# Optimization experiments

Hardware: AMD Instinct MI355X
Metric: run time of the kernel (lower is better)

Reference implementation:

```python
import jax, jax.numpy as jnp
import numpy as np


def setup_inputs() -> dict:
    key = jax.random.key(0)
    k1, k2 = jax.random.split(key)
    B, Lc, Lm, D = 8, 2048, 2048, 128
    context = jax.random.normal(k1, (B, Lc, D), dtype=jnp.float32)
    main = jax.random.normal(k2, (B, Lm, D), dtype=jnp.float32)
    return {"context": context, "main": main}


def reference(context, main):
    # weights[b,c,m] = sum_d context[b,c,d] * main[b,m,d]   (Keras dot axes=[2,2])
    weights = jnp.einsum("bcd,bmd->bcm", context, main)
    # K.softmax default axis=-1: normalize over the main-length axis m
    weights = jax.nn.softmax(weights, axis=-1)
    # dot([weights, context], axes=1): contract axis 1 (c) of both -> (B, Lm, D)
    weighted = jnp.einsum("bcm,bcd->bmd", weights, context)
    return main - weighted
```

## Files before the change

kernel.cpp:

```cpp
#include <hip/hip_runtime.h>


#define BATCH 8
#define L_SEQ 2048
#define DD 128
#define SHIFT 40.0f
#define LDA 136

typedef __attribute__((ext_vector_type(8))) short bf16x8;
typedef __attribute__((ext_vector_type(4))) short bf16x4;
typedef __attribute__((ext_vector_type(4))) float f32x4;
typedef __attribute__((ext_vector_type(16))) float f32x16;
typedef __attribute__((ext_vector_type(4))) unsigned int uint4v;

__device__ __forceinline__ short f2bf(float f) {
    unsigned u = __builtin_bit_cast(unsigned, f);
    return (short)((u + 0x8000u) >> 16);
}

__device__ __forceinline__ void gl2lds16(const short* g, short* l) {
    __builtin_amdgcn_global_load_lds(
        (const __attribute__((address_space(1))) unsigned int*)g,
        (__attribute__((address_space(3))) unsigned int*)l, 16, 0, 0);
}

__device__ __forceinline__ void waitv8() { asm volatile("s_waitcnt vmcnt(8)" ::: "memory"); }
__device__ __forceinline__ void waitv4() { asm volatile("s_waitcnt vmcnt(4)" ::: "memory"); }
__device__ __forceinline__ void waitv0() { asm volatile("s_waitcnt vmcnt(0)" ::: "memory"); }

template <int NT>
__device__ __forceinline__ void stage_tile(short* __restrict__ dst,
                                           const float* __restrict__ src,
                                           int nelts, int t) {
    for (int base = 0; base < nelts; base += NT * 8) {
        int flat = base + t * 8;
        const float4* p = (const float4*)(src + flat);
        float4 v0 = p[0];
        float4 v1 = p[1];
        bf16x8 s;
        s[0] = f2bf(v0.x); s[1] = f2bf(v0.y); s[2] = f2bf(v0.z); s[3] = f2bf(v0.w);
        s[4] = f2bf(v1.x); s[5] = f2bf(v1.y); s[6] = f2bf(v1.z); s[7] = f2bf(v1.w);
        int row = flat >> 7;
        int col = flat & 127;
        *(bf16x8*)&dst[row * LDA + col] = s;
    }
}

__global__ __launch_bounds__(256) void zero_kernel(float* __restrict__ p, int n) {
    int i = blockIdx.x * 256 + threadIdx.x;
    if (i < n) p[i] = 0.0f;
}


__global__ __launch_bounds__(256) void convert_kernel(const float* __restrict__ ctx,
                                                      const float* __restrict__ mn,
                                                      short* __restrict__ Cbf,
                                                      short* __restrict__ Mbf,
                                                      float* __restrict__ Lg) {
    int tid = blockIdx.x * 256 + threadIdx.x;
    if (tid < BATCH * L_SEQ) Lg[tid] = 0.0f;
    const int half = BATCH * L_SEQ * DD / 8;
    int id = tid;
    const float* src;
    short* dst;
    if (id < half) { src = ctx; dst = Cbf; }
    else           { id -= half; src = mn; dst = Mbf; }
    int row = id >> 4;
    int lc = id & 15;
    const float4* p = (const float4*)(src + ((size_t)row << 7) + lc * 8);
    float4 v0 = p[0];
    float4 v1 = p[1];
    bf16x8 s;
    s[0] = f2bf(v0.x); s[1] = f2bf(v0.y); s[2] = f2bf(v0.z); s[3] = f2bf(v0.w);
    s[4] = f2bf(v1.x); s[5] = f2bf(v1.y); s[6] = f2bf(v1.z); s[7] = f2bf(v1.w);
    int pc = (lc & 8) | ((lc ^ row) & 7);
    *(bf16x8*)&dst[((size_t)row << 7) + pc * 8] = s;
}

__global__ __launch_bounds__(256, 2) void stats_kernel(const short* __restrict__ Cbf,
                                                       const short* __restrict__ Mbf,
                                                       float* __restrict__ Lg) {
    __shared__ short Cs[128 * 128];
    __shared__ short Ms[2][64 * 128];

    int bid = blockIdx.x;
    int b  = bid & 7;
    int r2 = bid >> 3;
    int mc = r2 & 3;
    int ct = r2 >> 2;
    int t = threadIdx.x;
    int w = t >> 6;
    int l = t & 63;
    int a15 = l & 15;
    int q = l >> 4;
    int h = a15 & 7;
    int cw = (w & 1) * 64;
    int mw = (w >> 1) * 32;

    const short* gC = Cbf + ((size_t)(b * L_SEQ + ct * 128)) * DD;
    const short* gM = Mbf + ((size_t)(b * L_SEQ + mc * 512)) * DD;

    {
        #pragma unroll
        for (int ii = 0; ii < 8; ++ii) {
            int inst = w * 8 + ii;
            gl2lds16(gC + inst * 512 + l * 8, Cs + inst * 512);
        }
        #pragma unroll
        for (int ii = 0; ii < 4; ++ii) {
            int inst = w * 4 + ii;
            gl2lds16(gM + inst * 512 + l * 8, Ms[0] + inst * 512);
        }
        #pragma unroll
        for (int ii = 0; ii < 4; ++ii) {
            int inst = w * 4 + ii;
            gl2lds16(gM + (size_t)64 * DD + inst * 512 + l * 8, Ms[1] + inst * 512);
        }
    }

    waitv8();
    __builtin_amdgcn_s_barrier();
    __builtin_amdgcn_sched_barrier(0);

    bf16x8 af[4][4];
    #pragma unroll
    for (int ks = 0; ks < 4; ++ks) {
        int aoff = ((ks * 4 + q) ^ h) * 8;
        #pragma unroll
        for (int i = 0; i < 4; ++i)
            af[ks][i] = *(const bf16x8*)&Cs[(cw + i * 16 + a15) * 128 + aoff];
    }

    float ls[4][4] = {};

    for (int ms = 0; ms < 8; ++ms) {
        int bp = ms & 1;
        if (ms < 7) waitv4(); else waitv0();
        __builtin_amdgcn_s_barrier();
        __builtin_amdgcn_sched_barrier(0);

        f32x4 acc[4][2];
        #pragma unroll
        for (int i = 0; i < 4; ++i)
            #pragma unroll
            for (int j = 0; j < 2; ++j) {
                f32x4 z = {0.f, 0.f, 0.f, 0.f};
                acc[i][j] = z;
            }
        #pragma unroll
        for (int ks = 0; ks < 4; ++ks) {
            int aoff = ((ks * 4 + q) ^ h) * 8;
            bf16x8 bv[2];
            #pragma unroll
            for (int j = 0; j < 2; ++j)
                bv[j] = *(const bf16x8*)&Ms[bp][(mw + j * 16 + a15) * 128 + aoff];
            #pragma unroll
            for (int i = 0; i < 4; ++i)
                #pragma unroll
                for (int j = 0; j < 2; ++j)
                    acc[i][j] = __builtin_amdgcn_mfma_f32_16x16x32_bf16(af[ks][i], bv[j], acc[i][j], 0, 0, 0);
        }

        #pragma unroll
        for (int j = 0; j < 2; ++j)
            #pragma unroll
            for (int i = 0; i < 4; ++i)
                #pragma unroll
                for (int r = 0; r < 4; ++r)
                    ls[i][r] += __expf(acc[i][j][r] - SHIFT);

        __builtin_amdgcn_s_barrier();
        __builtin_amdgcn_sched_barrier(0);
        if (ms + 2 < 8) {
            #pragma unroll
            for (int ii = 0; ii < 4; ++ii) {
                int inst = w * 4 + ii;
                gl2lds16(gM + (size_t)(ms + 2) * 64 * DD + inst * 512 + l * 8,
                         Ms[bp] + inst * 512);
            }
        }
    }

    #pragma unroll
    for (int i = 0; i < 4; ++i)
        #pragma unroll
        for (int r = 0; r < 4; ++r) {
            float v = ls[i][r];
            v += __shfl_xor(v, 1);
            v += __shfl_xor(v, 2);
            v += __shfl_xor(v, 4);
            v += __shfl_xor(v, 8);
            ls[i][r] = v;
        }
    if (a15 == 0) {
        #pragma unroll
        for (int i = 0; i < 4; ++i) {
            int c = ct * 128 + cw + i * 16 + q * 4;
            #pragma unroll
            for (int r = 0; r < 4; ++r)
                atomicAdd(&Lg[(size_t)b * L_SEQ + c + r], ls[i][r]);
        }
    }
}

__global__ __launch_bounds__(256) void prep_kernel(const float* __restrict__ ctx,
                                                   const float* __restrict__ Lg,
                                                   short* __restrict__ CtL) {
    __shared__ short Ts[128 * LDA];
    __shared__ float invLs[128];

    int b = blockIdx.x >> 4;
    int cc = blockIdx.x & 15;
    int t = threadIdx.x;

    if (t < 128) invLs[t] = 1.0f / Lg[(size_t)b * L_SEQ + cc * 128 + t];
    __syncthreads();

    const float* src = ctx + ((size_t)(b * L_SEQ + cc * 128)) * DD;
    #pragma unroll
    for (int i = 0; i < 8; ++i) {
        int flat = i * 2048 + t * 8;
        int r = flat >> 7;
        int c = flat & 127;
        const float4* p = (const float4*)(src + flat);
        float4 v0 = p[0];
        float4 v1 = p[1];
        float il = invLs[r];
        bf16x8 s;
        s[0] = f2bf(v0.x * il); s[1] = f2bf(v0.y * il); s[2] = f2bf(v0.z * il); s[3] = f2bf(v0.w * il);
        s[4] = f2bf(v1.x * il); s[5] = f2bf(v1.y * il); s[6] = f2bf(v1.z * il); s[7] = f2bf(v1.w * il);
        *(bf16x8*)&Ts[r * LDA + c] = s;
    }
    __syncthreads();

    int d = t >> 1;
    int ch = (t & 1) * 64;
    int key = d & 7;
    #pragma unroll
    for (int i = 0; i < 8; ++i) {
        int c = ch + i * 8;
        bf16x8 v;
        #pragma unroll
        for (int j = 0; j < 8; ++j) v[j] = Ts[(c + j) * LDA + d];
        int pc = cc * 16 + (ch >> 3) + (i ^ key);
        *(bf16x8*)&CtL[((size_t)(b * DD + d)) * L_SEQ + pc * 8] = v;
    }
}

__global__ __launch_bounds__(512, 2) void attend_fused(const short* __restrict__ Cbf,
                                                       const short* __restrict__ Mbf,
                                                       const short* __restrict__ CtL,
                                                       const float* __restrict__ mn,
                                                       float* __restrict__ out) {
    __shared__ __align__(16) char smem[131072];

    int bid = blockIdx.x;
    int b = bid & 7;
    int mtile = bid >> 3;
    int t = threadIdx.x;
    int w = t >> 6;
    int l = t & 63;
    int la = l & 31;
    int hi = l >> 5;
    int mg = w >> 2;
    int ch = w & 3;

    int m_glob = mtile * 64 + mg * 32 + la;
    int key7 = la & 7;

    bf16x8 mf[8];
    {
        const short* mrow = Mbf + ((size_t)(b * L_SEQ + m_glob)) * DD;
        #pragma unroll
        for (int ks = 0; ks < 8; ++ks) {
            int lc = ks * 2 + hi;
            int pc = (lc & 8) | ((lc ^ key7) & 7);
            mf[ks] = *(const bf16x8*)&mrow[pc * 8];
        }
    }

    auto stage = [&](int cs, int p) {
        short* Cw = (short*)(smem + p * 65536);
        short* Tw = (short*)(smem + p * 65536 + 32768);
        const short* gC = Cbf + ((size_t)(b * L_SEQ + cs * 128)) * DD;
        #pragma unroll
        for (int ii = 0; ii < 4; ++ii) {
            int inst = w * 4 + ii;
            gl2lds16(gC + inst * 512 + l * 8, Cw + inst * 512);
        }
        const short* gT = CtL + (size_t)b * DD * L_SEQ + (size_t)cs * 128;
        #pragma unroll
        for (int ii = 0; ii < 4; ++ii) {
            int inst = w * 4 + ii;
            int row = inst * 4 + (l >> 4);
            gl2lds16(gT + (size_t)row * L_SEQ + (l & 15) * 8, Tw + inst * 512);
        }
    };

    f32x16 o[4];
    #pragma unroll
    for (int dg = 0; dg < 4; ++dg)
        #pragma unroll
        for (int r = 0; r < 16; ++r) o[dg][r] = 0.0f;

    stage(0, 0);
    stage(1, 1);

    for (int cs = 0; cs < 16; ++cs) {
        int p = cs & 1;
        if (cs < 15) waitv8(); else waitv0();
        __builtin_amdgcn_s_barrier();
        __builtin_amdgcn_sched_barrier(0);

        const short* Cw = (const short*)(smem + p * 65536);
        const short* Tw = (const short*)(smem + p * 65536 + 32768);

        f32x16 s;
        #pragma unroll
        for (int r = 0; r < 16; ++r) s[r] = 0.0f;
        int crow = ch * 32 + la;
        #pragma unroll
        for (int ks = 0; ks < 8; ++ks) {
            int lc = ks * 2 + hi;
            int pc = (lc & 8) | ((lc ^ key7) & 7);
            bf16x8 av = *(const bf16x8*)&Cw[crow * 128 + pc * 8];
            s = __builtin_amdgcn_mfma_f32_32x32x16_bf16(av, mf[ks], s, 0, 0, 0);
        }

        unsigned u[4][2];
        #pragma unroll
        for (int q = 0; q < 4; ++q)
            #pragma unroll
            for (int jj = 0; jj < 2; ++jj) {
                float e0 = __expf(s[q * 4 + jj * 2]     - SHIFT);
                float e1 = __expf(s[q * 4 + jj * 2 + 1] - SHIFT);
                u[q][jj] = ((unsigned)(unsigned short)f2bf(e1) << 16)
                         |  (unsigned)(unsigned short)f2bf(e0);
            }

        bf16x8 pa[2];
        #pragma unroll
        for (int ks2 = 0; ks2 < 2; ++ks2) {
            unsigned a0 = u[2 * ks2][0],     a1 = u[2 * ks2][1];
            unsigned b0 = u[2 * ks2 + 1][0], b1 = u[2 * ks2 + 1][1];
            unsigned a0p = (unsigned)__shfl_xor((int)a0, 32);
            unsigned a1p = (unsigned)__shfl_xor((int)a1, 32);
            unsigned b0p = (unsigned)__shfl_xor((int)b0, 32);
            unsigned b1p = (unsigned)__shfl_xor((int)b1, 32);
            uint4v pw;
            pw.x = hi ? b0p : a0;
            pw.y = hi ? b1p : a1;
            pw.z = hi ? b0  : a0p;
            pw.w = hi ? b1  : a1p;
            pa[ks2] = __builtin_bit_cast(bf16x8, pw);
        }

        #pragma unroll
        for (int dg = 0; dg < 4; ++dg) {
            int drow = dg * 32 + la;
            #pragma unroll
            for (int ks2 = 0; ks2 < 2; ++ks2) {
                int lc2 = ch * 4 + ks2 * 2 + hi;
                int pc2 = (lc2 & 8) | ((lc2 ^ key7) & 7);
                bf16x8 tv = *(const bf16x8*)&Tw[drow * 128 + pc2 * 8];
                o[dg] = __builtin_amdgcn_mfma_f32_32x32x16_bf16(tv, pa[ks2], o[dg], 0, 0, 0);
            }
        }

        __builtin_amdgcn_s_barrier();
        __builtin_amdgcn_sched_barrier(0);
        if (cs + 2 < 16) stage(cs + 2, p);
    }

    __syncthreads();
    float* red = (float*)smem;
    {
        float* base = red + w * 4096;
        #pragma unroll
        for (int dg = 0; dg < 4; ++dg)
            #pragma unroll
            for (int r = 0; r < 16; ++r) {
                int d = dg * 32 + (r & 3) + 8 * (r >> 2) + 4 * hi;
                base[d * 32 + la] = o[dg][r];
            }
    }
    __syncthreads();

    {
        int mg2 = t >> 8;
        int dq  = (t >> 5) & 7;
        int m   = t & 31;
        int m_out = mtile * 64 + mg2 * 32 + m;
        size_t gbase = ((size_t)(b * L_SEQ + m_out)) * DD + dq * 16;
        const float* r0 = red + (mg2 * 4 + 0) * 4096;
        const float* r1 = red + (mg2 * 4 + 1) * 4096;
        const float* r2 = red + (mg2 * 4 + 2) * 4096;
        const float* r3 = red + (mg2 * 4 + 3) * 4096;
        #pragma unroll
        for (int jq = 0; jq < 4; ++jq) {
            f32x4 v;
            #pragma unroll
            for (int e = 0; e < 4; ++e) {
                int idx = (dq * 16 + jq * 4 + e) * 32 + m;
                v[e] = r0[idx] + r1[idx] + r2[idx] + r3[idx];
            }
            f32x4 mv = *(const f32x4*)&mn[gbase + jq * 4];
            f32x4 ov;
            ov[0] = mv[0] - v[0]; ov[1] = mv[1] - v[1];
            ov[2] = mv[2] - v[2]; ov[3] = mv[3] - v[3];
            *(f32x4*)&out[gbase + jq * 4] = ov;
        }
    }
}


__global__ __launch_bounds__(256, 4) void stats_fb(const float* __restrict__ ctx,
                                                   const float* __restrict__ mn,
                                                   float* __restrict__ Lg) {
    __shared__ short Cs[64 * LDA];
    __shared__ short Ms[64 * LDA];

    int bid = blockIdx.x;
    int mc = bid & 3;
    int ct = (bid >> 2) & 31;
    int b  = bid >> 7;
    int t = threadIdx.x;
    int w = t >> 6;
    int l = t & 63;
    int a15 = l & 15;
    int q = l >> 4;

    stage_tile<256>(Cs, ctx + ((size_t)b * L_SEQ + ct * 64) * DD, 64 * DD, t);

    float ls[4] = {0.f, 0.f, 0.f, 0.f};
    for (int mt = 0; mt < 8; ++mt) {
        __syncthreads();
        int m0 = (mc * 8 + mt) * 64;
        stage_tile<256>(Ms, mn + ((size_t)b * L_SEQ + m0) * DD, 64 * DD, t);
        __syncthreads();

        f32x4 acc[4] = {{0.f,0.f,0.f,0.f},{0.f,0.f,0.f,0.f},{0.f,0.f,0.f,0.f},{0.f,0.f,0.f,0.f}};
        #pragma unroll
        for (int ks = 0; ks < 4; ++ks) {
            int k0 = ks * 32 + q * 8;
            bf16x8 a = *(const bf16x8*)&Cs[(w * 16 + a15) * LDA + k0];
            #pragma unroll
            for (int g = 0; g < 4; ++g) {
                bf16x8 bb = *(const bf16x8*)&Ms[(g * 16 + a15) * LDA + k0];
                acc[g] = __builtin_amdgcn_mfma_f32_16x16x32_bf16(a, bb, acc[g], 0, 0, 0);
            }
        }
        #pragma unroll
        for (int g = 0; g < 4; ++g)
            #pragma unroll
            for (int r = 0; r < 4; ++r)
                ls[r] += __expf(acc[g][r] - SHIFT);
    }

    #pragma unroll
    for (int r = 0; r < 4; ++r) {
        float v = ls[r];
        v += __shfl_xor(v, 1);
        v += __shfl_xor(v, 2);
        v += __shfl_xor(v, 4);
        v += __shfl_xor(v, 8);
        ls[r] = v;
    }
    if (a15 == 0) {
        int c = ct * 64 + w * 16 + q * 4;
        #pragma unroll
        for (int r = 0; r < 4; ++r)
            atomicAdd(&Lg[(size_t)b * L_SEQ + c + r], ls[r]);
    }
}

__global__ __launch_bounds__(1024, 4) void attend_fb(const float* __restrict__ ctx,
                                                     const float* __restrict__ mn,
                                                     const float* __restrict__ Lg,
                                                     float* __restrict__ out) {
    __shared__ short Mt[64 * LDA];
    __shared__ short Cs[128 * LDA];
    __shared__ short Ct[128 * LDA];
    __shared__ short Ps[64 * LDA];
    __shared__ float invLs[128];

    int bid = blockIdx.x;
    int mtile = bid & 31;
    int b = bid >> 5;
    int m0 = mtile * 64;
    int t = threadIdx.x;
    int w = t >> 6;
    int l = t & 63;
    int a15 = l & 15;
    int q = l >> 4;
    int mg = w & 3;
    int pg = w >> 2;

    stage_tile<1024>(Mt, mn + ((size_t)b * L_SEQ + m0) * DD, 64 * DD, t);

    f32x4 oacc[2] = {{0.f,0.f,0.f,0.f},{0.f,0.f,0.f,0.f}};

    for (int cs = 0; cs < 16; ++cs) {
        int c0 = cs * 128;
        __syncthreads();
        stage_tile<1024>(Cs, ctx + ((size_t)b * L_SEQ + c0) * DD, 128 * DD, t);
        if (t < 128) invLs[t] = 1.0f / Lg[(size_t)b * L_SEQ + c0 + t];
        __syncthreads();

        {
            int cc = t & 127;
            int d0 = (t >> 7) * 16;
            #pragma unroll
            for (int hh = 0; hh < 2; ++hh) {
                bf16x8 v = *(const bf16x8*)&Cs[cc * LDA + d0 + hh * 8];
                #pragma unroll
                for (int j = 0; j < 8; ++j)
                    Ct[(d0 + hh * 8 + j) * LDA + cc] = v[j];
            }
        }

        f32x4 sacc[2] = {{0.f,0.f,0.f,0.f},{0.f,0.f,0.f,0.f}};
        #pragma unroll
        for (int ks = 0; ks < 4; ++ks) {
            int k0 = ks * 32 + q * 8;
            bf16x8 a = *(const bf16x8*)&Mt[(mg * 16 + a15) * LDA + k0];
            #pragma unroll
            for (int g = 0; g < 2; ++g) {
                bf16x8 bb = *(const bf16x8*)&Cs[((pg * 2 + g) * 16 + a15) * LDA + k0];
                sacc[g] = __builtin_amdgcn_mfma_f32_16x16x32_bf16(a, bb, sacc[g], 0, 0, 0);
            }
        }
        #pragma unroll
        for (int g = 0; g < 2; ++g) {
            int cl = (pg * 2 + g) * 16 + a15;
            float il = invLs[cl];
            #pragma unroll
            for (int r = 0; r < 4; ++r) {
                float p = __expf(sacc[g][r] - SHIFT) * il;
                Ps[(mg * 16 + q * 4 + r) * LDA + cl] = f2bf(p);
            }
        }
        __syncthreads();

        #pragma unroll
        for (int ks = 0; ks < 4; ++ks) {
            int k0 = ks * 32 + q * 8;
            bf16x8 a = *(const bf16x8*)&Ps[(mg * 16 + a15) * LDA + k0];
            #pragma unroll
            for (int g = 0; g < 2; ++g) {
                bf16x8 bb = *(const bf16x8*)&Ct[((pg * 2 + g) * 16 + a15) * LDA + k0];
                oacc[g] = __builtin_amdgcn_mfma_f32_16x16x32_bf16(a, bb, oacc[g], 0, 0, 0);
            }
        }
    }

    #pragma unroll
    for (int g = 0; g < 2; ++g) {
        int dl = (pg * 2 + g) * 16 + a15;
        #pragma unroll
        for (int r = 0; r < 4; ++r) {
            int ml = mg * 16 + q * 4 + r;
            size_t idx = ((size_t)b * L_SEQ + m0 + ml) * DD + dl;
            out[idx] = mn[idx] - oacc[g][r];
        }
    }
}


extern "C" void kernel_launch(void* const* d_in, const int* in_sizes, int n_in,
                              void* d_out, int out_size, void* d_ws, size_t ws_size,
                              hipStream_t stream) {
    const float* ctx = (const float*)d_in[0];
    const float* mn  = (const float*)d_in[1];
    float* out = (float*)d_out;

    const size_t LG_BYTES = (size_t)BATCH * L_SEQ * sizeof(float);
    const size_t BF_BYTES = (size_t)BATCH * L_SEQ * DD * sizeof(short);
    const size_t NEED = LG_BYTES + 3 * BF_BYTES;

    float* Lg = (float*)d_ws;

    if (ws_size >= NEED) {
        short* Cbf = (short*)((char*)d_ws + LG_BYTES);
        short* Mbf = (short*)((char*)d_ws + LG_BYTES + BF_BYTES);
        short* CtL = (short*)((char*)d_ws + LG_BYTES + 2 * BF_BYTES);
        convert_kernel<<<2048, 256, 0, stream>>>(ctx, mn, Cbf, Mbf, Lg);
        stats_kernel<<<BATCH * 16 * 4, 256, 0, stream>>>(Cbf, Mbf, Lg);
        prep_kernel<<<BATCH * 16, 256, 0, stream>>>(ctx, Lg, CtL);
        attend_fused<<<BATCH * 32, 512, 0, stream>>>(Cbf, Mbf, CtL, mn, out);
    } else {
        int nL = BATCH * L_SEQ;
        zero_kernel<<<(nL + 255) / 256, 256, 0, stream>>>(Lg, nL);
        stats_fb<<<BATCH * 32 * 4, 256, 0, stream>>>(ctx, mn, Lg);
        attend_fb<<<BATCH * 32, 1024, 0, stream>>>(ctx, mn, Lg, out);
    }
}
```

Measured before the change: 119.1 us.

## Pre-swizzle scaled context into MFMA fragment order and load directly to registers

The prep kernel now writes the normalized, transposed context in per-lane MFMA fragment order, so the attend kernel reads its B-operand tiles straight from global memory into registers rather than staging them through LDS. The attend kernel is cut to 256 threads with 32 rows of main per block and twice as many blocks, and LDS use drops from 128KB to 64KB. This is meant to free LDS capacity and cut LDS traffic and occupancy pressure. In exchange, global fragment loads are issued inside the loop without double buffering, and every block now re-reads the full context.

Result: no change. 121.2 us (+1.8%).

```diff
diff --git a/kernel.cpp b/kernel.cpp
--- a/kernel.cpp
+++ b/kernel.cpp
@@ -205,7 +205,7 @@
 
 __global__ __launch_bounds__(256) void prep_kernel(const float* __restrict__ ctx,
                                                    const float* __restrict__ Lg,
-                                                   short* __restrict__ CtL) {
+                                                   short* __restrict__ CtLf) {
     __shared__ short Ts[128 * LDA];
     __shared__ float invLs[128];
 
@@ -233,26 +233,31 @@
     }
     __syncthreads();
 
-    int d = t >> 1;
-    int ch = (t & 1) * 64;
-    int key = d & 7;
     #pragma unroll
     for (int i = 0; i < 8; ++i) {
-        int c = ch + i * 8;
+        int slot = i * 256 + t;
+        int rec = slot >> 6;
+        int l2  = slot & 63;
+        int chh = rec >> 3;
+        int dgg = (rec >> 1) & 3;
+        int ks2 = rec & 1;
+        int la2 = l2 & 31;
+        int hi2 = l2 >> 5;
+        int d   = dgg * 32 + la2;
+        int c0  = (chh * 4 + ks2 * 2 + hi2) * 8;
         bf16x8 v;
         #pragma unroll
-        for (int j = 0; j < 8; ++j) v[j] = Ts[(c + j) * LDA + d];
-        int pc = cc * 16 + (ch >> 3) + (i ^ key);
-        *(bf16x8*)&CtL[((size_t)(b * DD + d)) * L_SEQ + pc * 8] = v;
-    }
-}
-
-__global__ __launch_bounds__(512, 2) void attend_fused(const short* __restrict__ Cbf,
+        for (int j = 0; j < 8; ++j) v[j] = Ts[(c0 + j) * LDA + d];
+        *(bf16x8*)&CtLf[((size_t)(b * 16 + cc) * 32 + rec) * 512 + l2 * 8] = v;
+    }
+}
+
+__global__ __launch_bounds__(256, 2) void attend_fused(const short* __restrict__ Cbf,
                                                        const short* __restrict__ Mbf,
-                                                       const short* __restrict__ CtL,
+                                                       const short* __restrict__ CtLf,
                                                        const float* __restrict__ mn,
                                                        float* __restrict__ out) {
-    __shared__ __align__(16) char smem[131072];
+    __shared__ __align__(16) char smem[65536];
 
     int bid = blockIdx.x;
     int b = bid & 7;
@@ -262,10 +267,9 @@
     int l = t & 63;
     int la = l & 31;
     int hi = l >> 5;
-    int mg = w >> 2;
-    int ch = w & 3;
-
-    int m_glob = mtile * 64 + mg * 32 + la;
+    int ch = w;
+
+    int m_glob = mtile * 32 + la;
     int key7 = la & 7;
 
     bf16x8 mf[8];
@@ -280,20 +284,12 @@
     }
 
     auto stage = [&](int cs, int p) {
-        short* Cw = (short*)(smem + p * 65536);
-        short* Tw = (short*)(smem + p * 65536 + 32768);
+        short* Cw = (short*)(smem + p * 32768);
         const short* gC = Cbf + ((size_t)(b * L_SEQ + cs * 128)) * DD;
         #pragma unroll
-        for (int ii = 0; ii < 4; ++ii) {
-            int inst = w * 4 + ii;
+        for (int ii = 0; ii < 8; ++ii) {
+            int inst = w * 8 + ii;
             gl2lds16(gC + inst * 512 + l * 8, Cw + inst * 512);
-        }
-        const short* gT = CtL + (size_t)b * DD * L_SEQ + (size_t)cs * 128;
-        #pragma unroll
-        for (int ii = 0; ii < 4; ++ii) {
-            int inst = w * 4 + ii;
-            int row = inst * 4 + (l >> 4);
-            gl2lds16(gT + (size_t)row * L_SEQ + (l & 15) * 8, Tw + inst * 512);
         }
     };
 
@@ -308,12 +304,19 @@
 
     for (int cs = 0; cs < 16; ++cs) {
         int p = cs & 1;
-        if (cs < 15) waitv8(); else waitv0();
+        waitv8();
         __builtin_amdgcn_s_barrier();
         __builtin_amdgcn_sched_barrier(0);
 
-        const short* Cw = (const short*)(smem + p * 65536);
-        const short* Tw = (const short*)(smem + p * 65536 + 32768);
+        const short* gF = CtLf + ((size_t)((b * 16 + cs) * 4 + ch) * 8) * 512 + l * 8;
+        bf16x8 tv[4][2];
+        #pragma unroll
+        for (int dg = 0; dg < 4; ++dg)
+            #pragma unroll
+            for (int ks2 = 0; ks2 < 2; ++ks2)
+                tv[dg][ks2] = *(const bf16x8*)&gF[(dg * 2 + ks2) * 512];
+
+        const short* Cw = (const short*)(smem + p * 32768);
 
         f32x16 s;
         #pragma unroll
@@ -356,16 +359,10 @@
         }
 
         #pragma unroll
-        for (int dg = 0; dg < 4; ++dg) {
-            int drow = dg * 32 + la;
-            #pragma unroll
-            for (int ks2 = 0; ks2 < 2; ++ks2) {
-                int lc2 = ch * 4 + ks2 * 2 + hi;
-                int pc2 = (lc2 & 8) | ((lc2 ^ key7) & 7);
-                bf16x8 tv = *(const bf16x8*)&Tw[drow * 128 + pc2 * 8];
-                o[dg] = __builtin_amdgcn_mfma_f32_32x32x16_bf16(tv, pa[ks2], o[dg], 0, 0, 0);
-            }
-        }
+        for (int dg = 0; dg < 4; ++dg)
+            #pragma unroll
+            for (int ks2 = 0; ks2 < 2; ++ks2)
+                o[dg] = __builtin_amdgcn_mfma_f32_32x32x16_bf16(tv[dg][ks2], pa[ks2], o[dg], 0, 0, 0);
 
         __builtin_amdgcn_s_barrier();
         __builtin_amdgcn_sched_barrier(0);
@@ -387,22 +384,16 @@
     __syncthreads();
 
     {
-        int mg2 = t >> 8;
-        int dq  = (t >> 5) & 7;
-        int m   = t & 31;
-        int m_out = mtile * 64 + mg2 * 32 + m;
-        size_t gbase = ((size_t)(b * L_SEQ + m_out)) * DD + dq * 16;
-        const float* r0 = red + (mg2 * 4 + 0) * 4096;
-        const float* r1 = red + (mg2 * 4 + 1) * 4096;
-        const float* r2 = red + (mg2 * 4 + 2) * 4096;
-        const float* r3 = red + (mg2 * 4 + 3) * 4096;
+        int m  = t & 31;
+        int dq = t >> 5;
+        size_t gbase = ((size_t)(b * L_SEQ + mtile * 32 + m)) * DD + dq * 16;
         #pragma unroll
         for (int jq = 0; jq < 4; ++jq) {
             f32x4 v;
             #pragma unroll
             for (int e = 0; e < 4; ++e) {
                 int idx = (dq * 16 + jq * 4 + e) * 32 + m;
-                v[e] = r0[idx] + r1[idx] + r2[idx] + r3[idx];
+                v[e] = red[idx] + red[4096 + idx] + red[8192 + idx] + red[12288 + idx];
             }
             f32x4 mv = *(const f32x4*)&mn[gbase + jq * 4];
             f32x4 ov;
@@ -581,13 +572,13 @@
     float* Lg = (float*)d_ws;
 
     if (ws_size >= NEED) {
-        short* Cbf = (short*)((char*)d_ws + LG_BYTES);
-        short* Mbf = (short*)((char*)d_ws + LG_BYTES + BF_BYTES);
-        short* CtL = (short*)((char*)d_ws + LG_BYTES + 2 * BF_BYTES);
+        short* Cbf  = (short*)((char*)d_ws + LG_BYTES);
+        short* Mbf  = (short*)((char*)d_ws + LG_BYTES + BF_BYTES);
+        short* CtLf = (short*)((char*)d_ws + LG_BYTES + 2 * BF_BYTES);
         convert_kernel<<<2048, 256, 0, stream>>>(ctx, mn, Cbf, Mbf, Lg);
         stats_kernel<<<BATCH * 16 * 4, 256, 0, stream>>>(Cbf, Mbf, Lg);
-        prep_kernel<<<BATCH * 16, 256, 0, stream>>>(ctx, Lg, CtL);
-        attend_fused<<<BATCH * 32, 512, 0, stream>>>(Cbf, Mbf, CtL, mn, out);
+        prep_kernel<<<BATCH * 16, 256, 0, stream>>>(ctx, Lg, CtLf);
+        attend_fused<<<BATCH * 64, 256, 0, stream>>>(Cbf, Mbf, CtLf, mn, out);
     } else {
         int nL = BATCH * L_SEQ;
         zero_kernel<<<(nL + 255) / 256, 256, 0, stream>>>(Lg, nL);
```
